# Kernel optimization log

Measured on AMD Instinct MI355X. Metric: run time of the kernel, lower is better.

The kernel has to match this reference:

```python
import jax, jax.numpy as jnp
import numpy as np

EP = 65536      # entity pairs (segments)
L = 8           # rows per span
N = EP * L      # total logit rows
C = 97          # relation classes (class 0 = threshold class)
BIG = 1e30


def setup_inputs() -> dict:
    key = jax.random.key(0)
    k1, k2 = jax.random.split(key)
    logits = jax.random.normal(k1, (N, C), dtype=jnp.float32)
    labels = (jax.random.uniform(k2, (EP, C)) < 0.03).astype(jnp.float32)
    starts = jnp.arange(EP, dtype=jnp.int32) * L
    pos = jnp.stack([starts, starts + L], axis=1)  # contiguous [st, en) spans
    return {"logits": logits, "labels": labels, "pos": pos}


def reference(logits, labels, pos):
    ep = pos.shape[0]
    n = logits.shape[0]
    # contiguous spans cover [0, N): row i belongs to segment j with end_j > i
    seg_ids = jnp.searchsorted(pos[:, 1], jnp.arange(n, dtype=pos.dtype), side="right")
    # ragged per-span max-reduction (single fused segment-max)
    e_logits = jax.ops.segment_max(logits, seg_ids, num_segments=ep)  # [EP, C]
    # threshold column taken from the first ep rows of raw logits
    e_logits = e_logits.at[:, 0].set(logits[:ep, 0])

    th_label = jnp.zeros_like(labels).at[:, 0].set(1.0)
    labels = labels.at[:, 0].set(0.0)
    p_mask = labels + th_label
    n_mask = 1.0 - labels

    loss1 = -(jax.nn.log_softmax(e_logits - (1.0 - p_mask) * BIG, axis=-1) * labels).sum(1)
    loss2 = -(jax.nn.log_softmax(e_logits - (1.0 - n_mask) * BIG, axis=-1) * th_label).sum(1)
    return (loss1 + loss2).mean()
```

## Files before the change

kernel.cpp:

```cpp
#include <hip/hip_runtime.h>
#include <math.h>

#define EP 65536
#define C 97
#define L 8
#define WAVES 4
#define ITERS 8
#define SEG_PER_BLOCK (WAVES * ITERS)
#define NBLOCKS (EP / SEG_PER_BLOCK)
#define SEG_FLOATS (L * C)

__device__ __forceinline__ float wred_max(float v) {
#pragma unroll
    for (int o = 32; o > 0; o >>= 1) v = fmaxf(v, __shfl_xor(v, o, 64));
    return v;
}
__device__ __forceinline__ float wred_sum(float v) {
#pragma unroll
    for (int o = 32; o > 0; o >>= 1) v += __shfl_xor(v, o, 64);
    return v;
}

__global__ __launch_bounds__(256) void atloss_main(
        const float* __restrict__ logits,
        const float* __restrict__ labels,
        const int*   __restrict__ pos,
        float*       __restrict__ partials) {
    const int tid  = threadIdx.x;
    const int w    = tid >> 6;
    const int lane = tid & 63;
    const int jbase = blockIdx.x * SEG_PER_BLOCK + w * ITERS;

    __shared__ float s_log[WAVES * SEG_FLOATS];
    __shared__ float s_loss[WAVES];
    float*  seg_s = s_log + w * SEG_FLOATS;
    float4* s4    = (float4*)seg_s;

    const int  c0   = lane;
    const int  c1   = lane + 64;
    const bool has1 = (c1 < C);

    int st_l = 0;
    if (lane < ITERS) st_l = pos[2 * (jbase + lane)];

    const int st0 = __shfl(st_l, 0, 64);
    const float4* g4 = (const float4*)(logits + (size_t)st0 * C);
    float4 A0 = g4[lane], A1 = g4[lane + 64], A2 = g4[lane + 128];
    float4 A3 = make_float4(0.f, 0.f, 0.f, 0.f);
    if (lane < 2) A3 = g4[192 + lane];
    size_t lbb = (size_t)jbase * C;
    float LB0 = labels[lbb + c0];
    float LB1 = has1 ? labels[lbb + c1] : 0.0f;
    float ETH = logits[(size_t)jbase * C];

    float wloss = 0.0f;

#pragma unroll
    for (int it = 0; it < ITERS; ++it) {
        const float4 B0 = A0, B1 = A1, B2 = A2, B3 = A3;
        const float  lb0r = LB0, lb1 = LB1, e_th = ETH;
        if (it + 1 < ITERS) {
            const int j1  = jbase + it + 1;
            const int st1 = __shfl(st_l, it + 1, 64);
            const float4* g4n = (const float4*)(logits + (size_t)st1 * C);
            A0 = g4n[lane]; A1 = g4n[lane + 64]; A2 = g4n[lane + 128];
            if (lane < 2) A3 = g4n[192 + lane];
            const size_t lbn = (size_t)j1 * C;
            LB0 = labels[lbn + c0];
            LB1 = has1 ? labels[lbn + c1] : 0.0f;
            ETH = logits[(size_t)j1 * C];
        }

        s4[lane] = B0; s4[lane + 64] = B1; s4[lane + 128] = B2;
        if (lane < 2) s4[192 + lane] = B3;

        float e0 = -INFINITY, e1 = -INFINITY;
#pragma unroll
        for (int r = 0; r < L; ++r) {
            e0 = fmaxf(e0, seg_s[r * C + c0]);
            if (has1) e1 = fmaxf(e1, seg_s[r * C + c1]);
        }
        if (lane == 0) e0 = e_th;
        const float lb0 = (lane == 0) ? 0.0f : lb0r;

        const bool pos0  = (c0 > 0) && (lb0 > 0.5f);
        const bool pos1  = has1 && (lb1 > 0.5f);
        const bool pset0 = (c0 == 0) || pos0;
        const bool nset0 = (lb0 < 0.5f);
        const bool nset1 = has1 && (lb1 < 0.5f);

        const float m  = wred_max(fmaxf(e0, has1 ? e1 : -INFINITY));
        const float x0 = expf(e0 - m);
        const float x1 = has1 ? expf(e1 - m) : 0.0f;

        const float sp   = wred_sum((pset0 ? x0 : 0.0f) + (pos1 ? x1 : 0.0f));
        const float sn   = wred_sum((nset0 ? x0 : 0.0f) + (nset1 ? x1 : 0.0f));
        const float npos = wred_sum((pos0 ? 1.0f : 0.0f) + (pos1 ? 1.0f : 0.0f));
        const float spos = wred_sum((pos0 ? e0 : 0.0f) + (pos1 ? e1 : 0.0f));

        const float lse_p = m + logf(sp);
        const float lse_n = m + logf(sn);
        wloss += npos * lse_p - spos + (lse_n - e_th);
    }

    if (lane == 0) s_loss[w] = wloss;
    __syncthreads();
    if (tid == 0) {
        float s = 0.0f;
#pragma unroll
        for (int k = 0; k < WAVES; ++k) s += s_loss[k];
        partials[blockIdx.x] = s;
    }
}

__global__ __launch_bounds__(256) void atloss_reduce(
        const float* __restrict__ partials, int n, float* __restrict__ out) {
    __shared__ double sh[256];
    double acc = 0.0;
    for (int i = threadIdx.x; i < n; i += 256) acc += (double)partials[i];
    sh[threadIdx.x] = acc;
    __syncthreads();
    for (int s = 128; s > 0; s >>= 1) {
        if (threadIdx.x < s) sh[threadIdx.x] += sh[threadIdx.x + s];
        __syncthreads();
    }
    if (threadIdx.x == 0) out[0] = (float)(sh[0] / (double)EP);
}

extern "C" void kernel_launch(void* const* d_in, const int* in_sizes, int n_in,
                              void* d_out, int out_size, void* d_ws, size_t ws_size,
                              hipStream_t stream) {
    const float* logits = (const float*)d_in[0];
    const float* labels = (const float*)d_in[1];
    const int*   pos    = (const int*)d_in[2];
    float* out      = (float*)d_out;
    float* partials = (float*)d_ws;

    atloss_main<<<NBLOCKS, 256, 0, stream>>>(logits, labels, pos, partials);
    atloss_reduce<<<1, 256, 0, stream>>>(partials, NBLOCKS, out);
}
```

Before: 49.08 us.

## Fuse final reduction via last-block atomic counter and simplify per-segment softmax

Removes the separate reduce kernel: each block writes its partial, bumps an atomic counter, and the last block to finish does the final double-precision sum. The per-segment math drops the max subtraction and uses fast __expf/__logf. Positive-label sums are now gathered with ballot plus readlane loops instead of extra wave-wide shuffle reductions. Skipping the max shift risks overflow for large logits, and a memset launch is added to reset the counter.

```diff
diff --git a/kernel.cpp b/kernel.cpp
--- a/kernel.cpp
+++ b/kernel.cpp
@@ -10,22 +10,22 @@
 #define NBLOCKS (EP / SEG_PER_BLOCK)
 #define SEG_FLOATS (L * C)
 
-__device__ __forceinline__ float wred_max(float v) {
-#pragma unroll
-    for (int o = 32; o > 0; o >>= 1) v = fmaxf(v, __shfl_xor(v, o, 64));
-    return v;
-}
-__device__ __forceinline__ float wred_sum(float v) {
+__device__ __forceinline__ float wsum(float v) {
 #pragma unroll
     for (int o = 32; o > 0; o >>= 1) v += __shfl_xor(v, o, 64);
     return v;
+}
+__device__ __forceinline__ float rdlane(float v, int l) {
+    return __int_as_float(__builtin_amdgcn_readlane(__float_as_int(v), l));
 }
 
 __global__ __launch_bounds__(256) void atloss_main(
         const float* __restrict__ logits,
         const float* __restrict__ labels,
         const int*   __restrict__ pos,
-        float*       __restrict__ partials) {
+        float*       __restrict__ partials,
+        unsigned int* __restrict__ counter,
+        float*       __restrict__ out) {
     const int tid  = threadIdx.x;
     const int w    = tid >> 6;
     const int lane = tid & 63;
@@ -33,6 +33,7 @@
 
     __shared__ float s_log[WAVES * SEG_FLOATS];
     __shared__ float s_loss[WAVES];
+    __shared__ int   s_last;
     float*  seg_s = s_log + w * SEG_FLOATS;
     float4* s4    = (float4*)seg_s;
 
@@ -58,7 +59,7 @@
 #pragma unroll
     for (int it = 0; it < ITERS; ++it) {
         const float4 B0 = A0, B1 = A1, B2 = A2, B3 = A3;
-        const float  lb0r = LB0, lb1 = LB1, e_th = ETH;
+        const float  lb0 = LB0, lb1 = LB1, eth = ETH;
         if (it + 1 < ITERS) {
             const int j1  = jbase + it + 1;
             const int st1 = __shfl(st_l, it + 1, 64);
@@ -74,57 +75,78 @@
         s4[lane] = B0; s4[lane + 64] = B1; s4[lane + 128] = B2;
         if (lane < 2) s4[192 + lane] = B3;
 
-        float e0 = -INFINITY, e1 = -INFINITY;
-#pragma unroll
-        for (int r = 0; r < L; ++r) {
-            e0 = fmaxf(e0, seg_s[r * C + c0]);
-            if (has1) e1 = fmaxf(e1, seg_s[r * C + c1]);
+        float e0, e1 = -INFINITY;
+        {
+            const float m01 = fmaxf(seg_s[0 * C + c0], seg_s[1 * C + c0]);
+            const float m23 = fmaxf(seg_s[2 * C + c0], seg_s[3 * C + c0]);
+            const float m45 = fmaxf(seg_s[4 * C + c0], seg_s[5 * C + c0]);
+            const float m67 = fmaxf(seg_s[6 * C + c0], seg_s[7 * C + c0]);
+            e0 = fmaxf(fmaxf(m01, m23), fmaxf(m45, m67));
         }
-        if (lane == 0) e0 = e_th;
-        const float lb0 = (lane == 0) ? 0.0f : lb0r;
+        if (has1) {
+            const float m01 = fmaxf(seg_s[0 * C + c1], seg_s[1 * C + c1]);
+            const float m23 = fmaxf(seg_s[2 * C + c1], seg_s[3 * C + c1]);
+            const float m45 = fmaxf(seg_s[4 * C + c1], seg_s[5 * C + c1]);
+            const float m67 = fmaxf(seg_s[6 * C + c1], seg_s[7 * C + c1]);
+            e1 = fmaxf(fmaxf(m01, m23), fmaxf(m45, m67));
+        }
+        if (lane == 0) e0 = eth;
 
-        const bool pos0  = (c0 > 0) && (lb0 > 0.5f);
-        const bool pos1  = has1 && (lb1 > 0.5f);
-        const bool pset0 = (c0 == 0) || pos0;
-        const bool nset0 = (lb0 < 0.5f);
-        const bool nset1 = has1 && (lb1 < 0.5f);
+        const float x0 = __expf(e0);
+        const float x1 = has1 ? __expf(e1) : 0.0f;
+        const float s_all = wsum(x0 + x1);
 
-        const float m  = wred_max(fmaxf(e0, has1 ? e1 : -INFINITY));
-        const float x0 = expf(e0 - m);
-        const float x1 = has1 ? expf(e1 - m) : 0.0f;
+        const bool p0 = (lane > 0) && (lb0 > 0.5f);
+        const bool p1 = has1 && (lb1 > 0.5f);
+        unsigned long long m0 = __ballot(p0);
+        unsigned long long m1 = __ballot(p1);
+        const float npos = (float)(__popcll(m0) + __popcll(m1));
 
-        const float sp   = wred_sum((pset0 ? x0 : 0.0f) + (pos1 ? x1 : 0.0f));
-        const float sn   = wred_sum((nset0 ? x0 : 0.0f) + (nset1 ? x1 : 0.0f));
-        const float npos = wred_sum((pos0 ? 1.0f : 0.0f) + (pos1 ? 1.0f : 0.0f));
-        const float spos = wred_sum((pos0 ? e0 : 0.0f) + (pos1 ? e1 : 0.0f));
+        float sp_pos = 0.0f, spos = 0.0f;
+        while (m0) {
+            const int p = __builtin_ctzll(m0); m0 &= m0 - 1;
+            sp_pos += rdlane(x0, p); spos += rdlane(e0, p);
+        }
+        while (m1) {
+            const int p = __builtin_ctzll(m1); m1 &= m1 - 1;
+            sp_pos += rdlane(x1, p); spos += rdlane(e1, p);
+        }
 
-        const float lse_p = m + logf(sp);
-        const float lse_n = m + logf(sn);
-        wloss += npos * lse_p - spos + (lse_n - e_th);
+        const float x_th = rdlane(x0, 0);
+        const float sp = x_th + sp_pos;
+        const float sn = s_all - sp_pos;
+        wloss += npos * __logf(sp) - spos + (__logf(sn) - eth);
     }
 
     if (lane == 0) s_loss[w] = wloss;
     __syncthreads();
     if (tid == 0) {
-        float s = 0.0f;
-#pragma unroll
-        for (int k = 0; k < WAVES; ++k) s += s_loss[k];
+        const float s = s_loss[0] + s_loss[1] + s_loss[2] + s_loss[3];
         partials[blockIdx.x] = s;
+        __threadfence();
+        const unsigned int n = __hip_atomic_fetch_add(
+            counter, 1u, __ATOMIC_ACQ_REL, __HIP_MEMORY_SCOPE_AGENT);
+        s_last = (n == NBLOCKS - 1);
     }
-}
+    __syncthreads();
 
-__global__ __launch_bounds__(256) void atloss_reduce(
-        const float* __restrict__ partials, int n, float* __restrict__ out) {
-    __shared__ double sh[256];
-    double acc = 0.0;
-    for (int i = threadIdx.x; i < n; i += 256) acc += (double)partials[i];
-    sh[threadIdx.x] = acc;
-    __syncthreads();
-    for (int s = 128; s > 0; s >>= 1) {
-        if (threadIdx.x < s) sh[threadIdx.x] += sh[threadIdx.x + s];
+    if (s_last) {
+        __shared__ double sh[256];
+        __threadfence();
+        double acc = 0.0;
+        for (int i = tid; i < NBLOCKS; i += 256) {
+            const float pv = __hip_atomic_load(&partials[i], __ATOMIC_RELAXED,
+                                               __HIP_MEMORY_SCOPE_AGENT);
+            acc += (double)pv;
+        }
+        sh[tid] = acc;
         __syncthreads();
+        for (int s = 128; s > 0; s >>= 1) {
+            if (tid < s) sh[tid] += sh[tid + s];
+            __syncthreads();
+        }
+        if (tid == 0) out[0] = (float)(sh[0] / (double)EP);
     }
-    if (threadIdx.x == 0) out[0] = (float)(sh[0] / (double)EP);
 }
 
 extern "C" void kernel_launch(void* const* d_in, const int* in_sizes, int n_in,
@@ -133,9 +155,12 @@
     const float* logits = (const float*)d_in[0];
     const float* labels = (const float*)d_in[1];
     const int*   pos    = (const int*)d_in[2];
-    float* out      = (float*)d_out;
-    float* partials = (float*)d_ws;
+    float* out = (float*)d_out;
 
-    atloss_main<<<NBLOCKS, 256, 0, stream>>>(logits, labels, pos, partials);
-    atloss_reduce<<<1, 256, 0, stream>>>(partials, NBLOCKS, out);
+    unsigned int* counter  = (unsigned int*)d_ws;
+    float*        partials = (float*)((char*)d_ws + 64);
+
+    hipMemsetAsync(counter, 0, sizeof(unsigned int), stream);
+    atloss_main<<<NBLOCKS, 256, 0, stream>>>(logits, labels, pos,
+                                             partials, counter, out);
 }
```

Result: slower. 151.9 us (+209.5%).
